# Optimization experiments

Measured on AMD Instinct MI355X. Metric: run time of the kernel, lower is better.

## Reference

```python
import jax, jax.numpy as jnp
import numpy as np

B, T, O, H, CTX, HOR = 32, 24, 128, 512, 256, 48
MAX_STEP = 2.0


def setup_inputs() -> dict:
    key = jax.random.key(0)
    ks = jax.random.split(key, 20)
    def lin(k, out_d, in_d):
        bound = 1.0 / np.sqrt(in_d)
        kw, kb = jax.random.split(k)
        W = jax.random.uniform(kw, (out_d, in_d), jnp.float32, -bound, bound)
        b = jax.random.uniform(kb, (out_d,), jnp.float32, -bound, bound)
        return W, b
    W_emb, b_emb = lin(ks[0], H, 2)
    W_ctx, b_ctx = lin(ks[1], H, CTX)
    Wi_enc, bi_enc = lin(ks[2], 3 * H, H)
    Wh_enc, bh_enc = lin(ks[3], 3 * H, H)
    Wi_cell, bi_cell = lin(ks[4], 3 * H, H)
    Wh_cell, bh_cell = lin(ks[5], 3 * H, H)
    W1, b1 = lin(ks[6], H, H)
    W2, b2 = lin(ks[7], 2, H)
    z_ctx = jax.random.normal(ks[8], (B, CTX), jnp.float32)
    traj_hist = jax.random.uniform(ks[9], (B, T, O, 2), jnp.float32) * 10.0
    return dict(z_ctx=z_ctx, traj_hist=traj_hist,
                W_emb=W_emb, b_emb=b_emb, W_ctx=W_ctx, b_ctx=b_ctx,
                Wi_enc=Wi_enc, Wh_enc=Wh_enc, bi_enc=bi_enc, bh_enc=bh_enc,
                Wi_cell=Wi_cell, Wh_cell=Wh_cell, bi_cell=bi_cell, bh_cell=bh_cell,
                W1=W1, b1=b1, W2=W2, b2=b2, horizon=HOR)


def _gru(h, x, Wi, Wh, bi, bh):
    # PyTorch GRU gate math: gates ordered (r, z, n)
    gi = x @ Wi.T + bi  # [N, 3H]
    gh = h @ Wh.T + bh
    ir, iz, inn = jnp.split(gi, 3, axis=-1)
    hr, hz, hn = jnp.split(gh, 3, axis=-1)
    r = jax.nn.sigmoid(ir + hr)
    z = jax.nn.sigmoid(iz + hz)
    n = jnp.tanh(inn + r * hn)
    return (1.0 - z) * n + z * h


def reference(z_ctx, traj_hist, W_emb, b_emb, W_ctx, b_ctx,
              Wi_enc, Wh_enc, bi_enc, bh_enc,
              Wi_cell, Wh_cell, bi_cell, bh_cell,
              W1, b1, W2, b2, horizon):
    b, t, o, _ = traj_hist.shape
    Hd = W_emb.shape[0]
    seq = traj_hist.transpose(0, 2, 1, 3).reshape(b * o, t, 2)  # [N, t, 2]
    emb = seq @ W_emb.T + b_emb  # [N, t, H]

    h0 = jnp.zeros((b * o, Hd), traj_hist.dtype)
    def enc_step(h, x):
        return _gru(h, x, Wi_enc, Wh_enc, bi_enc, bh_enc), None
    h, _ = jax.lax.scan(enc_step, h0, emb.transpose(1, 0, 2))

    ctx = z_ctx @ W_ctx.T + b_ctx                         # [b, H]
    ctx = jnp.repeat(ctx[:, None, :], o, axis=1).reshape(b * o, Hd)
    h = h + ctx

    state0 = seq[:, -1]  # [N, 2]
    def dec_step(carry, _):
        h, state = carry
        inp = state @ W_emb.T + b_emb
        h = _gru(h, inp, Wi_cell, Wh_cell, bi_cell, bh_cell)
        d = jax.nn.gelu(h @ W1.T + b1, approximate=False) @ W2.T + b2  # [N, 2]
        d = MAX_STEP * jnp.tanh(d / MAX_STEP)
        s = state + d
        state = jnp.stack([jnp.clip(s[..., 0], -90.0, 90.0),
                           jnp.mod(s[..., 1], 360.0)], axis=-1)
        return (h, state), state
    _, outs = jax.lax.scan(dec_step, (h, state0), None, length=horizon)
    # outs: [horizon, N, 2] -> [b, horizon, o, 2]
    return outs.transpose(1, 0, 2).reshape(b, o, horizon, 2).transpose(0, 2, 1, 3)
```

## Files before the change

### kernel.cpp

```cpp
#include <hip/hip_runtime.h>
#include <hip/hip_bf16.h>
#include <math.h>

#define BB 32
#define TT 24
#define OO 128
#define HH 512
#define CTXD 256
#define HOR 48
#define NN (BB*OO)
#define G3 (3*HH)
#define KS 17

typedef unsigned short ushortt;
typedef __attribute__((ext_vector_type(8))) short bf16x8;
typedef __attribute__((ext_vector_type(4))) float f32x4;

__device__ __forceinline__ ushortt f2bf(float x) {
    union { float f; unsigned u; } v; v.f = x;
    unsigned r = v.u + 0x7FFF + ((v.u >> 16) & 1);
    return (ushortt)(r >> 16);
}
__device__ __forceinline__ float bf2f(ushortt b) {
    union { unsigned u; float f; } v; v.u = ((unsigned)b) << 16;
    return v.f;
}
__device__ __forceinline__ void splitbf(float x, ushortt& hi, ushortt& lo) {
    hi = f2bf(x);
    lo = f2bf(x - bf2f(hi));
}
__device__ __forceinline__ float sigm(float x) { return 1.f / (1.f + __expf(-x)); }
__device__ __forceinline__ float tanh_fast(float x) {
    float xc = fminf(fmaxf(x, -10.f), 10.f);
    float e = __expf(2.f * xc);
    return (e - 1.f) / (e + 1.f);
}



#define STEP_LOADA(Ad, ksv) do { const unsigned ko = (unsigned)(ksv) * 512; \
  _Pragma("unroll") for (int m_ = 0; m_ < 4; m_++) { \
    Ad[m_*2+0] = *reinterpret_cast<const bf16x8*>(RAh + ao[m_] + ko); \
    Ad[m_*2+1] = *reinterpret_cast<const bf16x8*>(RAl + ao[m_] + ko); \
  } } while(0)
#define STEP_LOADB(Bd, ksv) do { const unsigned ko = (unsigned)(ksv) * 512; \
  _Pragma("unroll") for (int i_ = 0; i_ < 6; i_++) { \
    Bd[i_*2+0] = *reinterpret_cast<const bf16x8*>(Bh + bo[i_] + ko); \
    Bd[i_*2+1] = *reinterpret_cast<const bf16x8*>(Bl + bo[i_] + ko); \
  } } while(0)
#define STEP_MFMA(Av, Bv) do { \
  _Pragma("unroll") for (int m_ = 0; m_ < 4; m_++) \
  _Pragma("unroll") for (int i_ = 0; i_ < 6; i_++) \
    acc[m_][i_] = __builtin_amdgcn_mfma_f32_16x16x32_bf16(Av[m_*2+0], Bv[i_*2+0], acc[m_][i_], 0,0,0); \
  _Pragma("unroll") for (int m_ = 0; m_ < 4; m_++) \
  _Pragma("unroll") for (int i_ = 0; i_ < 6; i_++) \
    acc[m_][i_] = __builtin_amdgcn_mfma_f32_16x16x32_bf16(Av[m_*2+0], Bv[i_*2+1], acc[m_][i_], 0,0,0); \
  _Pragma("unroll") for (int m_ = 0; m_ < 4; m_++) \
  _Pragma("unroll") for (int i_ = 0; i_ < 6; i_++) \
    acc[m_][i_] = __builtin_amdgcn_mfma_f32_16x16x32_bf16(Av[m_*2+1], Bv[i_*2+0], acc[m_][i_], 0,0,0); \
  } while(0)

template<bool ENC>
__global__ __launch_bounds__(256, 1) void step_kernel(
    const ushortt* __restrict__ RAh, const ushortt* __restrict__ RAl,
    ushortt* __restrict__ WAh, ushortt* __restrict__ WAl,
    const ushortt* __restrict__ Bh, const ushortt* __restrict__ Bl,
    const float* __restrict__ U, const float* __restrict__ cin,
    const float* __restrict__ xsrc, int t, const float* __restrict__ ctx)
{
    __shared__ float hbuf[256 * 36];
    const int mb = blockIdx.x & 15;
    const int jb = blockIdx.x >> 4;
    const int w = threadIdx.x >> 6, lane = threadIdx.x & 63;
    const int quad = lane >> 4, l15 = lane & 15;
    const int mtg = mb * 16 + w * 4;

    f32x4 acc[4][6];
#pragma unroll
    for (int a = 0; a < 4; a++)
#pragma unroll
        for (int b = 0; b < 6; b++) acc[a][b] = (f32x4){0.f,0.f,0.f,0.f};

    unsigned ao[4], bo[6];
#pragma unroll
    for (int mt = 0; mt < 4; mt++) ao[mt] = (unsigned)(mtg + mt) * (KS*512) + lane * 8;
#pragma unroll
    for (int g = 0; g < 3; g++)
#pragma unroll
        for (int jt = 0; jt < 2; jt++)
            bo[g*2+jt] = (unsigned)(g*32 + jb*2 + jt) * (KS*512) + lane * 8;

    bf16x8 aC[8], bC[12], aN[8], bN[12];
    STEP_LOADA(aC, 0); STEP_LOADB(bC, 0);
#pragma unroll 1
    for (int ks = 0; ks < 16; ks += 2) {
        STEP_LOADA(aN, ks+1); STEP_LOADB(bN, ks+1);
        STEP_MFMA(aC, bC);
        STEP_LOADA(aC, ks+2); STEP_LOADB(bC, ks+2);
        STEP_MFMA(aN, bN);
    }
    STEP_MFMA(aC, bC);

    const int jlo = jb * 32;
    float u0[2], u1[2], cc[2];
#pragma unroll
    for (int jt = 0; jt < 2; jt++) {
        int j = jlo + jt*16 + l15;
        u0[jt] = U[(1024 + j) * 2];
        u1[jt] = U[(1024 + j) * 2 + 1];
        cc[jt] = cin[1024 + j];
    }
    float x0v[4][4], x1v[4][4];
#pragma unroll
    for (int mt = 0; mt < 4; mt++)
#pragma unroll
        for (int reg = 0; reg < 4; reg++) {
            int row = (mtg + mt) * 16 + quad * 4 + reg;
            const float* p;
            if (ENC) p = xsrc + (((size_t)(row >> 7) * TT + t) * OO + (row & 127)) * 2;
            else     p = xsrc + (size_t)row * 2;
            x0v[mt][reg] = p[0]; x1v[mt][reg] = p[1];
        }
#pragma unroll
    for (int mt = 0; mt < 4; mt++)
#pragma unroll
        for (int jt = 0; jt < 2; jt++) {
            int qk = jt*2 + (l15 >> 3), slot = l15 & 7;
#pragma unroll
            for (int reg = 0; reg < 4; reg++) {
                int row = (mtg + mt) * 16 + quad * 4 + reg;
                float pr = acc[mt][0*2+jt][reg];
                float pz = acc[mt][1*2+jt][reg];
                float hn = acc[mt][2*2+jt][reg];
                unsigned pos = ((unsigned)((mtg + mt) * KS + jb) * 64 + qk*16 + quad*4 + reg) * 8 + slot;
                float hold = bf2f(RAh[pos]) + bf2f(RAl[pos]);
                float inn = fmaf(x1v[mt][reg], u1[jt], fmaf(x0v[mt][reg], u0[jt], cc[jt]));
                float rg = sigm(pr), zg = sigm(pz);
                float nn = tanh_fast(inn + rg * hn);
                float h = (1.f - zg) * nn + zg * hold;
                if (ENC && t == TT - 1) h += ctx[(size_t)(row >> 7) * HH + jlo + jt*16 + l15];
                hbuf[(w*64 + mt*16 + quad*4 + reg) * 36 + jt*16 + l15] = h;
            }
        }
    __syncthreads();
#pragma unroll
    for (int rr = 0; rr < 4; rr++) {
        int fr = threadIdx.x + 256 * rr;
        int mt16 = fr >> 6, fl = fr & 63;
        int qk = fl >> 4, rloc = mt16 * 16 + (fl & 15);
        const float4 v0 = *reinterpret_cast<const float4*>(&hbuf[rloc * 36 + qk * 8]);
        const float4 v1 = *reinterpret_cast<const float4*>(&hbuf[rloc * 36 + qk * 8 + 4]);
        float src[8] = {v0.x, v0.y, v0.z, v0.w, v1.x, v1.y, v1.z, v1.w};
        bf16x8 hv, lv;
#pragma unroll
        for (int s = 0; s < 8; s++) {
            ushortt hi, lo; splitbf(src[s], hi, lo);
            hv[s] = (short)hi; lv[s] = (short)lo;
        }
        unsigned base = ((unsigned)((mb*16 + mt16) * KS + jb) * 64 + fl) * 8;
        *reinterpret_cast<bf16x8*>(WAh + base) = hv;
        *reinterpret_cast<bf16x8*>(WAl + base) = lv;
    }
    if (ENC && jb == 0) {
        int row = mb * 256 + threadIdx.x;
        int tn = (t < TT - 1) ? (t + 1) : (TT - 1);
        const float* p = xsrc + (((size_t)(row >> 7) * TT + tn) * OO + (row & 127)) * 2;
        ushortt h0, l0, h1, l1;
        splitbf(p[0], h0, l0); splitbf(p[1], h1, l1);
        unsigned xb = ((unsigned)((row >> 4) * KS + 16) * 64 + (row & 15)) * 8;
        WAh[xb + 0] = h0; WAl[xb + 0] = l0;
        WAh[xb + 1] = h1; WAl[xb + 1] = l1;
    }
}

#define HEAD_LOADA(Ad, ksv) do { const unsigned ko = (unsigned)(ksv) * 512; \
  _Pragma("unroll") for (int m_ = 0; m_ < 4; m_++) { \
    Ad[m_*2+0] = *reinterpret_cast<const bf16x8*>(Ah + hao[m_] + ko); \
    Ad[m_*2+1] = *reinterpret_cast<const bf16x8*>(Al + hao[m_] + ko); \
  } } while(0)
#define HEAD_LOADB(Bd, ksv) do { const unsigned ko = (unsigned)(ksv) * 512; \
  _Pragma("unroll") for (int n_ = 0; n_ < 2; n_++) { \
    Bd[n_*2+0] = *reinterpret_cast<const bf16x8*>(Bh + hbo[n_] + ko); \
    Bd[n_*2+1] = *reinterpret_cast<const bf16x8*>(Bl + hbo[n_] + ko); \
  } } while(0)
#define HEAD_MFMA(Av, Bv) do { \
  _Pragma("unroll") for (int m_ = 0; m_ < 4; m_++) \
  _Pragma("unroll") for (int n_ = 0; n_ < 2; n_++) { \
    acc[m_][n_] = __builtin_amdgcn_mfma_f32_16x16x32_bf16(Av[m_*2+0], Bv[n_*2+0], acc[m_][n_], 0,0,0); \
    acc[m_][n_] = __builtin_amdgcn_mfma_f32_16x16x32_bf16(Av[m_*2+0], Bv[n_*2+1], acc[m_][n_], 0,0,0); \
    acc[m_][n_] = __builtin_amdgcn_mfma_f32_16x16x32_bf16(Av[m_*2+1], Bv[n_*2+0], acc[m_][n_], 0,0,0); \
  } } while(0)

__global__ __launch_bounds__(256, 1) void head_kernel(
    ushortt* Ah, ushortt* Al,
    const ushortt* __restrict__ Bh, const ushortt* __restrict__ Bl,
    const float* __restrict__ W2, const float* __restrict__ b2,
    float* __restrict__ d, unsigned* __restrict__ ctr,
    float* state, float* __restrict__ out, int t)
{
    const int mb = blockIdx.x & 15;
    const int nb = blockIdx.x >> 4;
    const int w = threadIdx.x >> 6, lane = threadIdx.x & 63;
    const int quad = lane >> 4, l15 = lane & 15;
    const int mtg = mb * 16 + w * 4;

    f32x4 acc[4][2];
#pragma unroll
    for (int a = 0; a < 4; a++)
#pragma unroll
        for (int b = 0; b < 2; b++) acc[a][b] = (f32x4){0.f,0.f,0.f,0.f};

    unsigned hao[4], hbo[2];
#pragma unroll
    for (int mt = 0; mt < 4; mt++) hao[mt] = (unsigned)(mtg + mt) * (KS*512) + lane * 8;
#pragma unroll
    for (int nt = 0; nt < 2; nt++) hbo[nt] = (unsigned)(nb*2 + nt) * (KS*512) + lane * 8;

    bf16x8 aC[8], bC[4], aN[8], bN[4];
    HEAD_LOADA(aC, 0); HEAD_LOADB(bC, 0);
#pragma unroll 1
    for (int ks = 0; ks < 16; ks += 2) {
        HEAD_LOADA(aN, ks+1); HEAD_LOADB(bN, ks+1);
        HEAD_MFMA(aC, bC);
        HEAD_LOADA(aC, ks+2); HEAD_LOADB(bC, ks+2);
        HEAD_MFMA(aN, bN);
    }
    HEAD_MFMA(aC, bC);

    float w2a[2], w2b[2];
#pragma unroll
    for (int nt = 0; nt < 2; nt++) {
        int col = (nb*2 + nt) * 16 + l15;
        w2a[nt] = W2[col]; w2b[nt] = W2[HH + col];
    }
    float p0[4][4], p1[4][4];
#pragma unroll
    for (int mt = 0; mt < 4; mt++)
#pragma unroll
        for (int reg = 0; reg < 4; reg++) { p0[mt][reg] = 0.f; p1[mt][reg] = 0.f; }
#pragma unroll
    for (int mt = 0; mt < 4; mt++)
#pragma unroll
        for (int nt = 0; nt < 2; nt++)
#pragma unroll
            for (int reg = 0; reg < 4; reg++) {
                float v = acc[mt][nt][reg];
                v = 0.5f * v * (1.0f + erff(v * 0.70710678118654752440f));
                p0[mt][reg] = fmaf(v, w2a[nt], p0[mt][reg]);
                p1[mt][reg] = fmaf(v, w2b[nt], p1[mt][reg]);
            }
#pragma unroll
    for (int m = 1; m < 16; m <<= 1)
#pragma unroll
        for (int mt = 0; mt < 4; mt++)
#pragma unroll
            for (int reg = 0; reg < 4; reg++) {
                p0[mt][reg] += __shfl_xor(p0[mt][reg], m, 64);
                p1[mt][reg] += __shfl_xor(p1[mt][reg], m, 64);
            }
    if (l15 == 0) {
#pragma unroll
        for (int mt = 0; mt < 4; mt++)
#pragma unroll
            for (int reg = 0; reg < 4; reg++) {
                int row = (mtg + mt) * 16 + quad * 4 + reg;
                atomicAdd(&d[row * 2], p0[mt][reg]);
                atomicAdd(&d[row * 2 + 1], p1[mt][reg]);
            }
    }

    __syncthreads();
    __shared__ unsigned lastv;
    if (threadIdx.x == 0) lastv = atomicAdd(ctr, 1u);
    __syncthreads();
    if (lastv == 255) {
        __threadfence();
#pragma unroll 1
        for (int rr = 0; rr < 16; rr++) {
            int row = rr * 256 + threadIdx.x;
            float d0 = d[row * 2]     + b2[0];
            float d1 = d[row * 2 + 1] + b2[1];
            d0 = 2.0f * tanhf(d0 * 0.5f);
            d1 = 2.0f * tanhf(d1 * 0.5f);
            float s0 = state[row * 2] + d0;
            s0 = fminf(fmaxf(s0, -90.f), 90.f);
            float s1 = state[row * 2 + 1] + d1;
            float rrm = fmodf(s1, 360.f);
            if (rrm < 0.f) rrm += 360.f;
            state[row * 2] = s0; state[row * 2 + 1] = rrm;
            float* op = out + (((size_t)(row >> 7) * HOR + t) * OO + (row & 127)) * 2;
            op[0] = s0; op[1] = rrm;
            ushortt h0, l0, h1, l1;
            splitbf(s0, h0, l0); splitbf(rrm, h1, l1);
            unsigned xb = ((unsigned)((row >> 4) * KS + 16) * 64 + (row & 15)) * 8;
            Ah[xb + 0] = h0; Al[xb + 0] = l0;
            Ah[xb + 1] = h1; Al[xb + 1] = l1;
        }
    }
}

__global__ void fuse_kernel(const float* __restrict__ Wi_enc, const float* __restrict__ bi_enc,
                            const float* __restrict__ Wi_cell, const float* __restrict__ bi_cell,
                            const float* __restrict__ W_emb, const float* __restrict__ b_emb,
                            float* __restrict__ Ue, float* __restrict__ ce,
                            float* __restrict__ Ud, float* __restrict__ cd) {
    int idx = blockIdx.x * 256 + threadIdx.x;
    if (idx >= 2 * G3) return;
    int which = idx / G3, j = idx % G3;
    const float* Wi = which ? Wi_cell : Wi_enc;
    const float* bi = which ? bi_cell : bi_enc;
    float u0 = 0.f, u1 = 0.f, cc = bi[j];
    for (int k = 0; k < HH; k++) {
        float w = Wi[(size_t)j * HH + k];
        u0 = fmaf(w, W_emb[k * 2 + 0], u0);
        u1 = fmaf(w, W_emb[k * 2 + 1], u1);
        cc = fmaf(w, b_emb[k], cc);
    }
    float* Uo = which ? Ud : Ue;
    float* cv = which ? cd : ce;
    Uo[j * 2 + 0] = u0; Uo[j * 2 + 1] = u1; cv[j] = cc;
}

__global__ void pack_frag(const float* __restrict__ W, const float* __restrict__ bhv,
                          const float* __restrict__ U, const float* __restrict__ cin,
                          const float* __restrict__ b1,
                          ushortt* __restrict__ Fh, ushortt* __restrict__ Fl, int N) {
    int idx = blockIdx.x * 256 + threadIdx.x;
    if (idx >= N * KS * 4) return;
    int n = idx / (KS * 4);
    int rem = idx - n * (KS * 4);
    int ks = rem >> 2, quad = rem & 3;
    int nt = n >> 4, l15 = n & 15;
    ushortt hv[8], lv[8];
#pragma unroll
    for (int s = 0; s < 8; s++) {
        int k = ks * 32 + quad * 8 + s;
        float v = 0.f;
        if (k < 512) v = W[(size_t)n * 512 + k];
        else if (k == 512) v = (U && n < 1024) ? U[n * 2 + 0] : 0.f;
        else if (k == 513) v = (U && n < 1024) ? U[n * 2 + 1] : 0.f;
        else if (k == 514) v = U ? ((n < 1024) ? (cin[n] + bhv[n]) : bhv[n]) : b1[n];
        ushortt hi, lo; splitbf(v, hi, lo);
        hv[s] = hi; lv[s] = lo;
    }
    size_t pos = ((size_t)(nt * KS + ks) * 64 + quad * 16 + l15) * 8;
#pragma unroll
    for (int s = 0; s < 8; s++) { Fh[pos + s] = hv[s]; Fl[pos + s] = lv[s]; }
}

__global__ void ctx_kernel(const float* __restrict__ z, const float* __restrict__ Wc,
                           const float* __restrict__ bc, float* __restrict__ ctx) {
    int idx = blockIdx.x * 256 + threadIdx.x;
    int b = idx >> 9, j = idx & 511;
    float acc = bc[j];
    const float4* zp = (const float4*)(z + (size_t)b * CTXD);
    const float4* wp = (const float4*)(Wc + (size_t)j * CTXD);
    for (int k = 0; k < CTXD / 4; k++) {
        float4 a = zp[k], ww = wp[k];
        acc = fmaf(a.x, ww.x, fmaf(a.y, ww.y, fmaf(a.z, ww.z, fmaf(a.w, ww.w, acc))));
    }
    ctx[idx] = acc;
}

__global__ void init_kernel(const float* __restrict__ traj,
                            ushortt* __restrict__ Ah0, ushortt* __restrict__ Al0,
                            ushortt* __restrict__ Ah1, ushortt* __restrict__ Al1,
                            float* __restrict__ state, float* __restrict__ d,
                            unsigned* __restrict__ ctr) {
    int b = blockIdx.x;
    if (b < 1024) {
        int item = b * 256 + threadIdx.x;
        int mt = item >> 10, ks = (item >> 6) & 15, q4 = item & 63;
        size_t pos32 = ((size_t)(mt * KS + ks)) * 256 + q4 * 4;
        uint4 z = {0u,0u,0u,0u};
        *reinterpret_cast<uint4*>(((unsigned*)Ah0) + pos32) = z;
        *reinterpret_cast<uint4*>(((unsigned*)Al0) + pos32) = z;
    } else if (b < 1040) {
        int row = (b - 1024) * 256 + threadIdx.x;
        int bi = row >> 7, o = row & 127;
        const float* tp = traj + (((size_t)bi * TT + 0) * OO + o) * 2;
        ushortt xh0, xl0, xh1, xl1;
        splitbf(tp[0], xh0, xl0); splitbf(tp[1], xh1, xl1);
        for (int qk = 0; qk < 4; qk++)
            for (int slot = 0; slot < 8; slot++) {
                size_t p = (((size_t)(row >> 4) * KS + 16) * 64 + qk * 16 + (row & 15)) * 8 + slot;
                ushortt vh0 = 0, vl0 = 0, vh1 = 0;
                if (qk == 0 && slot == 0) { vh0 = xh0; vl0 = xl0; }
                else if (qk == 0 && slot == 1) { vh0 = xh1; vl0 = xl1; }
                else if (qk == 0 && slot == 2) { vh0 = 0x3F80; vh1 = 0x3F80; }
                Ah0[p] = vh0; Al0[p] = vl0; Ah1[p] = vh1; Al1[p] = 0;
            }
        const float* sp = traj + (((size_t)bi * TT + 23) * OO + o) * 2;
        state[row * 2] = sp[0]; state[row * 2 + 1] = sp[1];
    } else if (b < 1424) {
        int i = (b - 1040) * 256 + threadIdx.x;
        float4 z = {0.f,0.f,0.f,0.f};
        reinterpret_cast<float4*>(d)[i] = z;
    } else {
        if (threadIdx.x < 48) ctr[threadIdx.x] = 0u;
    }
}

extern "C" void kernel_launch(void* const* d_in, const int* in_sizes, int n_in,
                              void* d_out, int out_size, void* d_ws, size_t ws_size,
                              hipStream_t stream) {
    const float* z_ctx   = (const float*)d_in[0];
    const float* traj    = (const float*)d_in[1];
    const float* W_emb   = (const float*)d_in[2];
    const float* b_emb   = (const float*)d_in[3];
    const float* W_ctx   = (const float*)d_in[4];
    const float* b_ctx   = (const float*)d_in[5];
    const float* Wi_enc  = (const float*)d_in[6];
    const float* Wh_enc  = (const float*)d_in[7];
    const float* bi_enc  = (const float*)d_in[8];
    const float* bh_enc  = (const float*)d_in[9];
    const float* Wi_cell = (const float*)d_in[10];
    const float* Wh_cell = (const float*)d_in[11];
    const float* bi_cell = (const float*)d_in[12];
    const float* bh_cell = (const float*)d_in[13];
    const float* W1      = (const float*)d_in[14];
    const float* b1      = (const float*)d_in[15];
    const float* W2      = (const float*)d_in[16];
    const float* b2      = (const float*)d_in[17];
    float* out = (float*)d_out;

    char* ws = (char*)d_ws;
    size_t off = 0;
    auto alloc = [&](size_t bytes) { void* p = ws + off; off += (bytes + 255) & ~(size_t)255; return p; };
    const size_t hfrag = (size_t)256 * KS * 512 * 2;
    const size_t wfrag = (size_t)96  * KS * 512 * 2;
    const size_t w1frag = (size_t)32 * KS * 512 * 2;
    ushortt* Ah0 = (ushortt*)alloc(hfrag);
    ushortt* Al0 = (ushortt*)alloc(hfrag);
    ushortt* Ah1 = (ushortt*)alloc(hfrag);
    ushortt* Al1 = (ushortt*)alloc(hfrag);
    ushortt* WheH = (ushortt*)alloc(wfrag);
    ushortt* WheL = (ushortt*)alloc(wfrag);
    ushortt* WhdH = (ushortt*)alloc(wfrag);
    ushortt* WhdL = (ushortt*)alloc(wfrag);
    ushortt* W1H  = (ushortt*)alloc(w1frag);
    ushortt* W1L  = (ushortt*)alloc(w1frag);
    float*   state = (float*)alloc((size_t)NN * 2 * 4);
    float*   ctxb  = (float*)alloc((size_t)BB * HH * 4);
    float*   Ue    = (float*)alloc((size_t)G3 * 2 * 4);
    float*   ce    = (float*)alloc((size_t)G3 * 4);
    float*   Ud    = (float*)alloc((size_t)G3 * 2 * 4);
    float*   cd    = (float*)alloc((size_t)G3 * 4);
    float*   dbuf  = (float*)alloc((size_t)HOR * NN * 2 * 4);
    unsigned* ctr  = (unsigned*)alloc(HOR * 4);

    ushortt* bufAh[2] = {Ah0, Ah1};
    ushortt* bufAl[2] = {Al0, Al1};

    fuse_kernel<<<(2 * G3 + 255) / 256, 256, 0, stream>>>(Wi_enc, bi_enc, Wi_cell, bi_cell,
                                                          W_emb, b_emb, Ue, ce, Ud, cd);
    ctx_kernel<<<(BB * HH) / 256, 256, 0, stream>>>(z_ctx, W_ctx, b_ctx, ctxb);
    pack_frag<<<(G3 * KS * 4 + 255) / 256, 256, 0, stream>>>(Wh_enc, bh_enc, Ue, ce, nullptr, WheH, WheL, G3);
    pack_frag<<<(G3 * KS * 4 + 255) / 256, 256, 0, stream>>>(Wh_cell, bh_cell, Ud, cd, nullptr, WhdH, WhdL, G3);
    pack_frag<<<(HH * KS * 4 + 255) / 256, 256, 0, stream>>>(W1, nullptr, nullptr, nullptr, b1, W1H, W1L, HH);
    init_kernel<<<1425, 256, 0, stream>>>(traj, Ah0, Al0, Ah1, Al1, state, dbuf, ctr);

    for (int t = 0; t < TT; t++) {
        int rp = t & 1, wp = (t + 1) & 1;
        step_kernel<true><<<256, 256, 0, stream>>>(bufAh[rp], bufAl[rp], bufAh[wp], bufAl[wp],
                                                   WheH, WheL, Ue, ce, traj, t, ctxb);
    }
    for (int t = 0; t < HOR; t++) {
        int s = TT + t;
        int rp = s & 1, wp = (s + 1) & 1;
        step_kernel<false><<<256, 256, 0, stream>>>(bufAh[rp], bufAl[rp], bufAh[wp], bufAl[wp],
                                                    WhdH, WhdL, Ud, cd, state, t, nullptr);
        head_kernel<<<256, 256, 0, stream>>>(bufAh[wp], bufAl[wp], W1H, W1L, W2, b2,
                                             dbuf + (size_t)t * NN * 2, ctr + t, state, out, t);
    }
}
```

Baseline: 4.020 ms.

## Halve row tiles per block to launch 512 blocks and parallelize fuse reduction

The step and head kernels now give each wave 2 row tiles instead of 4 and launch 512 blocks instead of 256, with launch bounds raised to 2 blocks per CU. This fills more of the MI355X's CUs, which 256 blocks per step left partly idle. The price is that each B-fragment of the weights is reloaded by twice as many blocks, so weight traffic per step goes up. The fuse_kernel also switches from a serial per-thread dot product to a per-wavefront strided reduction with shuffles, a one-time setup cost.

```diff
diff --git a/kernel.cpp b/kernel.cpp
--- a/kernel.cpp
+++ b/kernel.cpp
@@ -37,9 +37,8 @@
 }
 
 
-
 #define STEP_LOADA(Ad, ksv) do { const unsigned ko = (unsigned)(ksv) * 512; \
-  _Pragma("unroll") for (int m_ = 0; m_ < 4; m_++) { \
+  _Pragma("unroll") for (int m_ = 0; m_ < 2; m_++) { \
     Ad[m_*2+0] = *reinterpret_cast<const bf16x8*>(RAh + ao[m_] + ko); \
     Ad[m_*2+1] = *reinterpret_cast<const bf16x8*>(RAl + ao[m_] + ko); \
   } } while(0)
@@ -49,48 +48,48 @@
     Bd[i_*2+1] = *reinterpret_cast<const bf16x8*>(Bl + bo[i_] + ko); \
   } } while(0)
 #define STEP_MFMA(Av, Bv) do { \
-  _Pragma("unroll") for (int m_ = 0; m_ < 4; m_++) \
+  _Pragma("unroll") for (int m_ = 0; m_ < 2; m_++) \
   _Pragma("unroll") for (int i_ = 0; i_ < 6; i_++) \
     acc[m_][i_] = __builtin_amdgcn_mfma_f32_16x16x32_bf16(Av[m_*2+0], Bv[i_*2+0], acc[m_][i_], 0,0,0); \
-  _Pragma("unroll") for (int m_ = 0; m_ < 4; m_++) \
+  _Pragma("unroll") for (int m_ = 0; m_ < 2; m_++) \
   _Pragma("unroll") for (int i_ = 0; i_ < 6; i_++) \
     acc[m_][i_] = __builtin_amdgcn_mfma_f32_16x16x32_bf16(Av[m_*2+0], Bv[i_*2+1], acc[m_][i_], 0,0,0); \
-  _Pragma("unroll") for (int m_ = 0; m_ < 4; m_++) \
+  _Pragma("unroll") for (int m_ = 0; m_ < 2; m_++) \
   _Pragma("unroll") for (int i_ = 0; i_ < 6; i_++) \
     acc[m_][i_] = __builtin_amdgcn_mfma_f32_16x16x32_bf16(Av[m_*2+1], Bv[i_*2+0], acc[m_][i_], 0,0,0); \
   } while(0)
 
 template<bool ENC>
-__global__ __launch_bounds__(256, 1) void step_kernel(
+__global__ __launch_bounds__(256, 2) void step_kernel(
     const ushortt* __restrict__ RAh, const ushortt* __restrict__ RAl,
     ushortt* __restrict__ WAh, ushortt* __restrict__ WAl,
     const ushortt* __restrict__ Bh, const ushortt* __restrict__ Bl,
     const float* __restrict__ U, const float* __restrict__ cin,
     const float* __restrict__ xsrc, int t, const float* __restrict__ ctx)
 {
-    __shared__ float hbuf[256 * 36];
-    const int mb = blockIdx.x & 15;
-    const int jb = blockIdx.x >> 4;
+    __shared__ float hbuf[128 * 36];
+    const int mb = blockIdx.x & 31;
+    const int jb = blockIdx.x >> 5;
     const int w = threadIdx.x >> 6, lane = threadIdx.x & 63;
     const int quad = lane >> 4, l15 = lane & 15;
-    const int mtg = mb * 16 + w * 4;
-
-    f32x4 acc[4][6];
-#pragma unroll
-    for (int a = 0; a < 4; a++)
+    const int mtg = mb * 8 + w * 2;
+
+    f32x4 acc[2][6];
+#pragma unroll
+    for (int a = 0; a < 2; a++)
 #pragma unroll
         for (int b = 0; b < 6; b++) acc[a][b] = (f32x4){0.f,0.f,0.f,0.f};
 
-    unsigned ao[4], bo[6];
-#pragma unroll
-    for (int mt = 0; mt < 4; mt++) ao[mt] = (unsigned)(mtg + mt) * (KS*512) + lane * 8;
+    unsigned ao[2], bo[6];
+#pragma unroll
+    for (int mt = 0; mt < 2; mt++) ao[mt] = (unsigned)(mtg + mt) * (KS*512) + lane * 8;
 #pragma unroll
     for (int g = 0; g < 3; g++)
 #pragma unroll
         for (int jt = 0; jt < 2; jt++)
             bo[g*2+jt] = (unsigned)(g*32 + jb*2 + jt) * (KS*512) + lane * 8;
 
-    bf16x8 aC[8], bC[12], aN[8], bN[12];
+    bf16x8 aC[4], bC[12], aN[4], bN[12];
     STEP_LOADA(aC, 0); STEP_LOADB(bC, 0);
 #pragma unroll 1
     for (int ks = 0; ks < 16; ks += 2) {
@@ -110,9 +109,9 @@
         u1[jt] = U[(1024 + j) * 2 + 1];
         cc[jt] = cin[1024 + j];
     }
-    float x0v[4][4], x1v[4][4];
-#pragma unroll
-    for (int mt = 0; mt < 4; mt++)
+    float x0v[2][4], x1v[2][4];
+#pragma unroll
+    for (int mt = 0; mt < 2; mt++)
 #pragma unroll
         for (int reg = 0; reg < 4; reg++) {
             int row = (mtg + mt) * 16 + quad * 4 + reg;
@@ -122,7 +121,7 @@
             x0v[mt][reg] = p[0]; x1v[mt][reg] = p[1];
         }
 #pragma unroll
-    for (int mt = 0; mt < 4; mt++)
+    for (int mt = 0; mt < 2; mt++)
 #pragma unroll
         for (int jt = 0; jt < 2; jt++) {
             int qk = jt*2 + (l15 >> 3), slot = l15 & 7;
@@ -139,15 +138,15 @@
                 float nn = tanh_fast(inn + rg * hn);
                 float h = (1.f - zg) * nn + zg * hold;
                 if (ENC && t == TT - 1) h += ctx[(size_t)(row >> 7) * HH + jlo + jt*16 + l15];
-                hbuf[(w*64 + mt*16 + quad*4 + reg) * 36 + jt*16 + l15] = h;
+                hbuf[(w*32 + mt*16 + quad*4 + reg) * 36 + jt*16 + l15] = h;
             }
         }
     __syncthreads();
 #pragma unroll
-    for (int rr = 0; rr < 4; rr++) {
+    for (int rr = 0; rr < 2; rr++) {
         int fr = threadIdx.x + 256 * rr;
-        int mt16 = fr >> 6, fl = fr & 63;
-        int qk = fl >> 4, rloc = mt16 * 16 + (fl & 15);
+        int mt8 = fr >> 6, fl = fr & 63;
+        int qk = fl >> 4, rloc = mt8 * 16 + (fl & 15);
         const float4 v0 = *reinterpret_cast<const float4*>(&hbuf[rloc * 36 + qk * 8]);
         const float4 v1 = *reinterpret_cast<const float4*>(&hbuf[rloc * 36 + qk * 8 + 4]);
         float src[8] = {v0.x, v0.y, v0.z, v0.w, v1.x, v1.y, v1.z, v1.w};
@@ -157,12 +156,12 @@
             ushortt hi, lo; splitbf(src[s], hi, lo);
             hv[s] = (short)hi; lv[s] = (short)lo;
         }
-        unsigned base = ((unsigned)((mb*16 + mt16) * KS + jb) * 64 + fl) * 8;
+        unsigned base = ((unsigned)((mb*8 + mt8) * KS + jb) * 64 + fl) * 8;
         *reinterpret_cast<bf16x8*>(WAh + base) = hv;
         *reinterpret_cast<bf16x8*>(WAl + base) = lv;
     }
-    if (ENC && jb == 0) {
-        int row = mb * 256 + threadIdx.x;
+    if (ENC && jb == 0 && threadIdx.x < 128) {
+        int row = mb * 128 + threadIdx.x;
         int tn = (t < TT - 1) ? (t + 1) : (TT - 1);
         const float* p = xsrc + (((size_t)(row >> 7) * TT + tn) * OO + (row & 127)) * 2;
         ushortt h0, l0, h1, l1;
@@ -174,7 +173,7 @@
 }
 
 #define HEAD_LOADA(Ad, ksv) do { const unsigned ko = (unsigned)(ksv) * 512; \
-  _Pragma("unroll") for (int m_ = 0; m_ < 4; m_++) { \
+  _Pragma("unroll") for (int m_ = 0; m_ < 2; m_++) { \
     Ad[m_*2+0] = *reinterpret_cast<const bf16x8*>(Ah + hao[m_] + ko); \
     Ad[m_*2+1] = *reinterpret_cast<const bf16x8*>(Al + hao[m_] + ko); \
   } } while(0)
@@ -184,39 +183,39 @@
     Bd[n_*2+1] = *reinterpret_cast<const bf16x8*>(Bl + hbo[n_] + ko); \
   } } while(0)
 #define HEAD_MFMA(Av, Bv) do { \
-  _Pragma("unroll") for (int m_ = 0; m_ < 4; m_++) \
+  _Pragma("unroll") for (int m_ = 0; m_ < 2; m_++) \
   _Pragma("unroll") for (int n_ = 0; n_ < 2; n_++) { \
     acc[m_][n_] = __builtin_amdgcn_mfma_f32_16x16x32_bf16(Av[m_*2+0], Bv[n_*2+0], acc[m_][n_], 0,0,0); \
     acc[m_][n_] = __builtin_amdgcn_mfma_f32_16x16x32_bf16(Av[m_*2+0], Bv[n_*2+1], acc[m_][n_], 0,0,0); \
     acc[m_][n_] = __builtin_amdgcn_mfma_f32_16x16x32_bf16(Av[m_*2+1], Bv[n_*2+0], acc[m_][n_], 0,0,0); \
   } } while(0)
 
-__global__ __launch_bounds__(256, 1) void head_kernel(
+__global__ __launch_bounds__(256, 2) void head_kernel(
     ushortt* Ah, ushortt* Al,
     const ushortt* __restrict__ Bh, const ushortt* __restrict__ Bl,
     const float* __restrict__ W2, const float* __restrict__ b2,
     float* __restrict__ d, unsigned* __restrict__ ctr,
     float* state, float* __restrict__ out, int t)
 {
-    const int mb = blockIdx.x & 15;
-    const int nb = blockIdx.x >> 4;
+    const int mb = blockIdx.x & 31;
+    const int nb = blockIdx.x >> 5;
     const int w = threadIdx.x >> 6, lane = threadIdx.x & 63;
     const int quad = lane >> 4, l15 = lane & 15;
-    const int mtg = mb * 16 + w * 4;
-
-    f32x4 acc[4][2];
-#pragma unroll
-    for (int a = 0; a < 4; a++)
+    const int mtg = mb * 8 + w * 2;
+
+    f32x4 acc[2][2];
+#pragma unroll
+    for (int a = 0; a < 2; a++)
 #pragma unroll
         for (int b = 0; b < 2; b++) acc[a][b] = (f32x4){0.f,0.f,0.f,0.f};
 
-    unsigned hao[4], hbo[2];
-#pragma unroll
-    for (int mt = 0; mt < 4; mt++) hao[mt] = (unsigned)(mtg + mt) * (KS*512) + lane * 8;
+    unsigned hao[2], hbo[2];
+#pragma unroll
+    for (int mt = 0; mt < 2; mt++) hao[mt] = (unsigned)(mtg + mt) * (KS*512) + lane * 8;
 #pragma unroll
     for (int nt = 0; nt < 2; nt++) hbo[nt] = (unsigned)(nb*2 + nt) * (KS*512) + lane * 8;
 
-    bf16x8 aC[8], bC[4], aN[8], bN[4];
+    bf16x8 aC[4], bC[4], aN[4], bN[4];
     HEAD_LOADA(aC, 0); HEAD_LOADB(bC, 0);
 #pragma unroll 1
     for (int ks = 0; ks < 16; ks += 2) {
@@ -233,13 +232,13 @@
         int col = (nb*2 + nt) * 16 + l15;
         w2a[nt] = W2[col]; w2b[nt] = W2[HH + col];
     }
-    float p0[4][4], p1[4][4];
-#pragma unroll
-    for (int mt = 0; mt < 4; mt++)
+    float p0[2][4], p1[2][4];
+#pragma unroll
+    for (int mt = 0; mt < 2; mt++)
 #pragma unroll
         for (int reg = 0; reg < 4; reg++) { p0[mt][reg] = 0.f; p1[mt][reg] = 0.f; }
 #pragma unroll
-    for (int mt = 0; mt < 4; mt++)
+    for (int mt = 0; mt < 2; mt++)
 #pragma unroll
         for (int nt = 0; nt < 2; nt++)
 #pragma unroll
@@ -252,7 +251,7 @@
 #pragma unroll
     for (int m = 1; m < 16; m <<= 1)
 #pragma unroll
-        for (int mt = 0; mt < 4; mt++)
+        for (int mt = 0; mt < 2; mt++)
 #pragma unroll
             for (int reg = 0; reg < 4; reg++) {
                 p0[mt][reg] += __shfl_xor(p0[mt][reg], m, 64);
@@ -260,7 +259,7 @@
             }
     if (l15 == 0) {
 #pragma unroll
-        for (int mt = 0; mt < 4; mt++)
+        for (int mt = 0; mt < 2; mt++)
 #pragma unroll
             for (int reg = 0; reg < 4; reg++) {
                 int row = (mtg + mt) * 16 + quad * 4 + reg;
@@ -273,7 +272,7 @@
     __shared__ unsigned lastv;
     if (threadIdx.x == 0) lastv = atomicAdd(ctr, 1u);
     __syncthreads();
-    if (lastv == 255) {
+    if (lastv == 511) {
         __threadfence();
 #pragma unroll 1
         for (int rr = 0; rr < 16; rr++) {
@@ -299,26 +298,38 @@
     }
 }
 
-__global__ void fuse_kernel(const float* __restrict__ Wi_enc, const float* __restrict__ bi_enc,
-                            const float* __restrict__ Wi_cell, const float* __restrict__ bi_cell,
-                            const float* __restrict__ W_emb, const float* __restrict__ b_emb,
-                            float* __restrict__ Ue, float* __restrict__ ce,
-                            float* __restrict__ Ud, float* __restrict__ cd) {
-    int idx = blockIdx.x * 256 + threadIdx.x;
-    if (idx >= 2 * G3) return;
-    int which = idx / G3, j = idx % G3;
+__global__ __launch_bounds__(256) void fuse_kernel(
+    const float* __restrict__ Wi_enc, const float* __restrict__ bi_enc,
+    const float* __restrict__ Wi_cell, const float* __restrict__ bi_cell,
+    const float* __restrict__ W_emb, const float* __restrict__ b_emb,
+    float* __restrict__ Ue, float* __restrict__ ce,
+    float* __restrict__ Ud, float* __restrict__ cd) {
+    int w = threadIdx.x >> 6, lane = threadIdx.x & 63;
+    int gidx = blockIdx.x * 4 + w;
+    int which = gidx >= G3;
+    int j = gidx - which * G3;
     const float* Wi = which ? Wi_cell : Wi_enc;
     const float* bi = which ? bi_cell : bi_enc;
-    float u0 = 0.f, u1 = 0.f, cc = bi[j];
-    for (int k = 0; k < HH; k++) {
-        float w = Wi[(size_t)j * HH + k];
-        u0 = fmaf(w, W_emb[k * 2 + 0], u0);
-        u1 = fmaf(w, W_emb[k * 2 + 1], u1);
-        cc = fmaf(w, b_emb[k], cc);
-    }
-    float* Uo = which ? Ud : Ue;
-    float* cv = which ? cd : ce;
-    Uo[j * 2 + 0] = u0; Uo[j * 2 + 1] = u1; cv[j] = cc;
+    float u0 = 0.f, u1 = 0.f, cc = 0.f;
+#pragma unroll
+    for (int i = 0; i < 8; i++) {
+        int k = i * 64 + lane;
+        float wv = Wi[(size_t)j * HH + k];
+        u0 = fmaf(wv, W_emb[2*k],   u0);
+        u1 = fmaf(wv, W_emb[2*k+1], u1);
+        cc = fmaf(wv, b_emb[k],     cc);
+    }
+#pragma unroll
+    for (int m = 1; m < 64; m <<= 1) {
+        u0 += __shfl_xor(u0, m, 64);
+        u1 += __shfl_xor(u1, m, 64);
+        cc += __shfl_xor(cc, m, 64);
+    }
+    if (lane == 0) {
+        float* Uo = which ? Ud : Ue;
+        float* cv = which ? cd : ce;
+        Uo[j * 2 + 0] = u0; Uo[j * 2 + 1] = u1; cv[j] = cc + bi[j];
+    }
 }
 
 __global__ void pack_frag(const float* __restrict__ W, const float* __restrict__ bhv,
@@ -452,8 +463,8 @@
     ushortt* bufAh[2] = {Ah0, Ah1};
     ushortt* bufAl[2] = {Al0, Al1};
 
-    fuse_kernel<<<(2 * G3 + 255) / 256, 256, 0, stream>>>(Wi_enc, bi_enc, Wi_cell, bi_cell,
-                                                          W_emb, b_emb, Ue, ce, Ud, cd);
+    fuse_kernel<<<768, 256, 0, stream>>>(Wi_enc, bi_enc, Wi_cell, bi_cell,
+                                         W_emb, b_emb, Ue, ce, Ud, cd);
     ctx_kernel<<<(BB * HH) / 256, 256, 0, stream>>>(z_ctx, W_ctx, b_ctx, ctxb);
     pack_frag<<<(G3 * KS * 4 + 255) / 256, 256, 0, stream>>>(Wh_enc, bh_enc, Ue, ce, nullptr, WheH, WheL, G3);
     pack_frag<<<(G3 * KS * 4 + 255) / 256, 256, 0, stream>>>(Wh_cell, bh_cell, Ud, cd, nullptr, WhdH, WhdL, G3);
@@ -462,15 +473,15 @@
 
     for (int t = 0; t < TT; t++) {
         int rp = t & 1, wp = (t + 1) & 1;
-        step_kernel<true><<<256, 256, 0, stream>>>(bufAh[rp], bufAl[rp], bufAh[wp], bufAl[wp],
+        step_kernel<true><<<512, 256, 0, stream>>>(bufAh[rp], bufAl[rp], bufAh[wp], bufAl[wp],
                                                    WheH, WheL, Ue, ce, traj, t, ctxb);
     }
     for (int t = 0; t < HOR; t++) {
         int s = TT + t;
         int rp = s & 1, wp = (s + 1) & 1;
-        step_kernel<false><<<256, 256, 0, stream>>>(bufAh[rp], bufAl[rp], bufAh[wp], bufAl[wp],
+        step_kernel<false><<<512, 256, 0, stream>>>(bufAh[rp], bufAl[rp], bufAh[wp], bufAl[wp],
                                                     WhdH, WhdL, Ud, cd, state, t, nullptr);
-        head_kernel<<<256, 256, 0, stream>>>(bufAh[wp], bufAl[wp], W1H, W1L, W2, b2,
+        head_kernel<<<512, 256, 0, stream>>>(bufAh[wp], bufAl[wp], W1H, W1L, W2, b2,
                                              dbuf + (size_t)t * NN * 2, ctr + t, state, out, t);
     }
 }
```

Measured after the change: 3.501 ms. 1.15x faster.
